# Kernel tuning notes

Measured on AMD Instinct MI355X. Metric: run time of the kernel, lower is better.

The kernel has to match this reference:

```python
import jax, jax.numpy as jnp
import numpy as np

N, R, E, H, F = 50000, 6, 32768, 256, 16
NH, HD = 8, 32
EPS_LN = 1e-5

def _ln(x, g, b):
    mu = x.mean(-1, keepdims=True)
    var = ((x - mu) ** 2).mean(-1, keepdims=True)
    return (x - mu) * jax.lax.rsqrt(var + EPS_LN) * g + b

def setup_inputs() -> dict:
    key = jax.random.key(0)
    ks = jax.random.split(key, 32)
    s = lambda i, shape, scale=0.05: jax.random.normal(ks[i], shape, jnp.float32) * scale
    return {
        'x': jax.random.normal(ks[0], (N, H), jnp.float32),
        'edge_index': jax.random.randint(ks[1], (R, 2, E), 0, N, jnp.int32),
        'edge_attr': jax.random.normal(ks[2], (R, E, F), jnp.float32),
        'Wq': s(3, (R, H, H)), 'bq': s(4, (R, H)),
        'Wk': s(5, (R, H + F, H)), 'bk': s(6, (R, H)),
        'Wv': s(7, (R, H + F, H)), 'bv': s(8, (R, H)),
        'prior': jnp.ones((R, NH), jnp.float32),
        'Wm': s(9, (R, H, H)), 'bm': s(10, (R, H)),
        'W_ir1': s(11, (R * H, H)), 'b_ir1': s(12, (H,)),
        'W_ir2': s(13, (H, R)), 'b_ir2': s(14, (R,)),
        'Wmp': s(15, (3, H, H)), 'bmp': s(16, (3, H)),
        'Wa1': s(17, (H, H // 2)), 'ba1': s(18, (H // 2,)),
        'Wa2': s(19, (H // 2, 1)),
        'g_meta': jnp.ones((H,), jnp.float32), 'b_meta': jnp.zeros((H,), jnp.float32),
        'Wc': s(20, (2 * H, H)), 'bc': s(21, (H,)),
        'g_out': jnp.ones((H,), jnp.float32), 'b_out': jnp.zeros((H,), jnp.float32),
    }

def _block(x, edge_index, edge_attr, Wq, bq, Wk, bk, Wv, bv, prior, Wm, bm,
           W_ir1, b_ir1, W_ir2, b_ir2, Wmp, bmp, Wa1, ba1, Wa2, g_meta, b_meta,
           Wc, bc, g_out, b_out):
    def rel_layer(eidx, eattr, wq, bq_, wk, bk_, wv, bv_, pr, wm, bm_):
        src, dst = eidx[0], eidx[1]
        q = x @ wq + bq_                                  # [N,H]
        kv_in = jnp.concatenate([x[src], eattr], -1)      # [E,H+F]
        k = (kv_in @ wk + bk_).reshape(E, NH, HD)
        v = (kv_in @ wv + bv_).reshape(E, NH, HD)
        qe = q[dst].reshape(E, NH, HD)
        scores = (qe * k).sum(-1) / np.sqrt(HD) * pr      # [E,NH]
        m = jax.ops.segment_max(scores, dst, num_segments=N)
        ex = jnp.exp(scores - m[dst])
        denom = jax.ops.segment_sum(ex, dst, num_segments=N)
        w = ex / (denom[dst] + 1e-16)
        wv_flat = (w[..., None] * v).reshape(E, H)
        agg = jax.ops.segment_sum(wv_flat, dst, num_segments=N)  # [N,H]
        return jax.nn.gelu(agg @ wm + bm_, approximate=False)

    rel_out = jax.vmap(rel_layer)(edge_index, edge_attr, Wq, bq, Wk, bk, Wv, bv,
                                  prior, Wm, bm)          # [R,N,H]

    all_rel = jnp.transpose(rel_out, (1, 0, 2)).reshape(N, R * H)
    h = jax.nn.gelu(all_rel @ W_ir1 + b_ir1, approximate=False)
    inter_w = jax.nn.softmax(h @ W_ir2 + b_ir2, axis=-1)  # [N,R]
    inter_agg = jnp.einsum('nr,rnh->nh', inter_w, rel_out)

    # meta-paths: 0=entangle(ENTANGLE=2,SWAP=3) 1=control(CONTROL=4,ROTATION=0) 2=local(PAULI=1,TEMPORAL=5)
    paths = jnp.stack([rel_out[2] + rel_out[3], rel_out[4] + rel_out[0],
                       rel_out[1] + rel_out[5]], axis=1)  # [N,3,H]
    stacked = jnp.einsum('nph,phk->npk', paths, Wmp) + bmp
    attn = jax.nn.softmax((jnp.tanh(stacked @ Wa1 + ba1) @ Wa2).squeeze(-1), axis=1)
    meta = _ln((attn[..., None] * stacked).sum(1), g_meta, b_meta)

    combined = jax.nn.gelu(jnp.concatenate([inter_agg, meta], -1) @ Wc + bc,
                           approximate=False)
    return _ln(x + combined, g_out, b_out)

def reference(x, edge_index, edge_attr, Wq, bq, Wk, bk, Wv, bv, prior, Wm, bm,
              W_ir1, b_ir1, W_ir2, b_ir2, Wmp, bmp, Wa1, ba1, Wa2, g_meta, b_meta,
              Wc, bc, g_out, b_out):
    return _block(x, edge_index, edge_attr, Wq, bq, Wk, bk, Wv, bv, prior, Wm, bm,
                  W_ir1, b_ir1, W_ir2, b_ir2, Wmp, bmp, Wa1, ba1, Wa2,
                  g_meta, b_meta, Wc, bc, g_out, b_out)
```

## Files before the change

kernel.cpp:

```cpp
#include <hip/hip_runtime.h>
#include <hip/hip_bf16.h>

typedef __hip_bfloat16 bf16;
typedef __attribute__((ext_vector_type(8))) short short8;
typedef __attribute__((ext_vector_type(4))) float f32x4;

#define NN 50000
#define RR 6
#define EE 32768
#define HH 256
#define FF 16
#define NHEAD 8
#define KVP 320

struct __align__(8) bf16x4 { bf16 v[4]; };

__device__ __forceinline__ float b2f(bf16 v) { return __bfloat162float(v); }
__device__ __forceinline__ bf16 f2b(float v) { return __float2bfloat16(v); }
__device__ __forceinline__ short f2s(float f) { bf16 b = f2b(f); return __builtin_bit_cast(short, b); }
__device__ __forceinline__ float s2f(short s) { return b2f(__builtin_bit_cast(bf16, s)); }
__device__ __forceinline__ float gelu_f(float x) { return 0.5f * x * (1.0f + erff(x * 0.7071067811865476f)); }

__device__ __forceinline__ void gl2lds16(const void* g, void* l) {
  __builtin_amdgcn_global_load_lds(
      (const __attribute__((address_space(1))) unsigned int*)g,
      (__attribute__((address_space(3))) unsigned int*)l, 16, 0, 0);
}

__global__ void zero_k(uint4* __restrict__ p, int n16)
{
  const uint4 z = make_uint4(0u, 0u, 0u, 0u);
  for (int i = blockIdx.x * blockDim.x + threadIdx.x; i < n16; i += gridDim.x * blockDim.x)
    p[i] = z;
}

__global__ void cvt_k(const float* __restrict__ in, bf16* __restrict__ out, int n4)
{
  const int i = blockIdx.x * 256 + threadIdx.x;
  if (i >= n4) return;
  const float4 f = ((const float4*)in)[i];
  bf16x4 o; o.v[0] = f2b(f.x); o.v[1] = f2b(f.y); o.v[2] = f2b(f.z); o.v[3] = f2b(f.w);
  ((bf16x4*)out)[i] = o;
}

__global__ void tconv_k(const float* __restrict__ in, bf16* __restrict__ out,
                        int K, int NC, int Kp, long izs, long ozs)
{
  __shared__ float t[32][33];
  in  += (size_t)blockIdx.z * izs;
  out += (size_t)blockIdx.z * ozs;
  const int kb = blockIdx.x * 32, nb = blockIdx.y * 32;
  const int tx = threadIdx.x & 31, ty = threadIdx.x >> 5;
  for (int i = ty; i < 32; i += 8) {
    const int k = kb + i, n = nb + tx;
    t[i][tx] = (k < K && n < NC) ? in[(size_t)k * NC + n] : 0.f;
  }
  __syncthreads();
  for (int i = ty; i < 32; i += 8) {
    const int n = nb + i, k = kb + tx;
    if (n < NC && k < Kp) out[(size_t)n * Kp + k] = f2b(t[tx][i]);
  }
}

__global__ void bkv_k(const float* __restrict__ bk, const float* __restrict__ bv,
                      float* __restrict__ bkv)
{
  const int i = blockIdx.x * 256 + threadIdx.x;
  if (i >= RR * 512) return;
  const int r = i >> 9, c = i & 511;
  bkv[i] = (c < 256) ? bk[r * 256 + c] : bv[r * 256 + (c - 256)];
}

__global__ void copyslot_k(const bf16* __restrict__ tmp, bf16* __restrict__ slot)
{
  const int i = blockIdx.x * 256 + threadIdx.x;
  if (i >= NN * 32) return;
  const int n = i >> 5, c = (i & 31) * 8;
  *(short8*)(slot + (size_t)n * 1536 + c) = *(const short8*)(tmp + (size_t)n * 256 + c);
}

template<int ASRC, int ACT, int ZMODE, typename TO>
__global__ __launch_bounds__(256) void mm_k(
    const void* __restrict__ Av, const bf16* __restrict__ A2, int lda,
    const int* __restrict__ src, const bf16* __restrict__ eab,
    const float* __restrict__ dnm,
    const bf16* __restrict__ Bt, const float* __restrict__ bias,
    const float* __restrict__ wa2, TO* __restrict__ C, int ldc,
    float* __restrict__ logits, int M, int K, int z0)
{
  __shared__ short lA[128 * 64];
  __shared__ short lB[128 * 64];
  const int tid = threadIdx.x;
  const int w = tid >> 6, l = tid & 63;
  const int col0 = blockIdx.x << 7;
  const int row0 = blockIdx.y << 7;
  const bf16* Ab = (const bf16*)Av;
  const bf16* A2b = A2;
  const bf16* Btz = Bt;
  const float* biasz = bias;
  TO* Cz = C;
  float* lg = logits;
  if constexpr (ZMODE == 1) {
    const int slots3[3] = {2, 4, 1};
    Ab = (const bf16*)Av + slots3[blockIdx.z] * 256;
    lg = logits + (size_t)blockIdx.z * M;
  } else if constexpr (ZMODE == 3) {
    const int r1s[3] = {2, 4, 1}, r2s[3] = {3, 0, 5};
    const int z = blockIdx.z + z0;
    Ab  = (const bf16*)Av + (size_t)r1s[z] * 256;
    A2b = A2 + (size_t)r2s[z] * 256;
    Btz = Bt + (size_t)z * 256 * K;
    biasz = bias + z * 256;
    Cz = C + (size_t)blockIdx.z * (size_t)M * 256;
  }
  const int wm = (w >> 1) << 6, wn = (w & 1) << 6;
  const int lane15 = l & 15, kq = l >> 4;

  f32x4 acc[4][4] = {};

  for (int k0 = 0; k0 < K; k0 += 64) {
#pragma unroll
    for (int i = 0; i < 4; ++i) {
      const int idx = (w * 4 + i) * 64 + l;
      const int row = idx >> 3, cg = idx & 7;
      const int scg = cg ^ (row & 7);
      const int r = min(row0 + row, M - 1);
      const int kc = k0 + scg * 8;
      if constexpr (ASRC == 0) {
        gl2lds16(Ab + (size_t)r * lda + kc, &lA[idx * 8]);
      } else if constexpr (ASRC == 2) {
        const short8 u  = *(const short8*)(Ab  + (size_t)r * lda + kc);
        const short8 v2 = *(const short8*)(A2b + (size_t)r * lda + kc);
        short8 s;
#pragma unroll
        for (int j = 0; j < 8; ++j) s[j] = f2s(s2f(u[j]) + s2f(v2[j]));
        *(short8*)&lA[idx * 8] = s;
      } else if constexpr (ASRC == 3) {
        short8 s;
        if (kc < HH) {
          s = *(const short8*)((const bf16*)Av + (size_t)src[r] * HH + kc);
        } else if (kc < HH + FF) {
          s = *(const short8*)(eab + (size_t)r * FF + (kc - HH));
        } else {
#pragma unroll
          for (int j = 0; j < 8; ++j) s[j] = 0;
        }
        *(short8*)&lA[idx * 8] = s;
      } else {
        const float* p = (const float*)Av + (size_t)r * lda + kc;
        const float4 f0 = *(const float4*)p;
        const float4 f1 = *(const float4*)(p + 4);
        const float iv = 1.0f / (dnm[r * NHEAD + (kc >> 5)] + 1e-16f);
        short8 s;
        s[0] = f2s(f0.x * iv); s[1] = f2s(f0.y * iv); s[2] = f2s(f0.z * iv); s[3] = f2s(f0.w * iv);
        s[4] = f2s(f1.x * iv); s[5] = f2s(f1.y * iv); s[6] = f2s(f1.z * iv); s[7] = f2s(f1.w * iv);
        *(short8*)&lA[idx * 8] = s;
      }
    }
#pragma unroll
    for (int i = 0; i < 4; ++i) {
      const int idx = (w * 4 + i) * 64 + l;
      const int row = idx >> 3, cg = idx & 7;
      const int scg = cg ^ (row & 7);
      gl2lds16(Btz + (size_t)(col0 + row) * K + k0 + scg * 8, &lB[idx * 8]);
    }
    __syncthreads();
#pragma unroll
    for (int kk = 0; kk < 64; kk += 32) {
      short8 af[4], bfr[4];
#pragma unroll
      for (int t = 0; t < 4; ++t) {
        const int ra = wm + t * 16 + lane15;
        const int ca = ((kk >> 3) + kq) ^ (ra & 7);
        af[t] = *(const short8*)&lA[ra * 64 + ca * 8];
        const int rb = wn + t * 16 + lane15;
        const int cb = ((kk >> 3) + kq) ^ (rb & 7);
        bfr[t] = *(const short8*)&lB[rb * 64 + cb * 8];
      }
#pragma unroll
      for (int ti = 0; ti < 4; ++ti)
#pragma unroll
        for (int tj = 0; tj < 4; ++tj)
          acc[ti][tj] = __builtin_amdgcn_mfma_f32_16x16x32_bf16(af[ti], bfr[tj], acc[ti][tj], 0, 0, 0);
    }
    __syncthreads();
  }

  if constexpr (ZMODE != 1) {
#pragma unroll
    for (int ti = 0; ti < 4; ++ti) {
#pragma unroll
      for (int reg = 0; reg < 4; ++reg) {
        const int row = row0 + wm + ti * 16 + kq * 4 + reg;
        if (row >= M) continue;
#pragma unroll
        for (int tj = 0; tj < 4; ++tj) {
          const int col = col0 + wn + tj * 16 + lane15;
          float v = acc[ti][tj][reg] + biasz[col];
          if constexpr (ACT == 1) v = gelu_f(v);
          if constexpr (sizeof(TO) == 2) Cz[(size_t)row * ldc + col] = (TO)f2b(v);
          else                           Cz[(size_t)row * ldc + col] = (TO)v;
        }
      }
    }
  } else {
#pragma unroll
    for (int ti = 0; ti < 4; ++ti) {
#pragma unroll
      for (int reg = 0; reg < 4; ++reg) {
        float part = 0.f;
#pragma unroll
        for (int tj = 0; tj < 4; ++tj) {
          const int col = col0 + wn + tj * 16 + lane15;
          part += tanhf(acc[ti][tj][reg] + biasz[col]) * wa2[col];
        }
#pragma unroll
        for (int off = 8; off > 0; off >>= 1) part += __shfl_xor(part, off, 64);
        const int row = row0 + wm + ti * 16 + kq * 4 + reg;
        if (lane15 == 0 && row < M) atomicAdd(&lg[row], part);
      }
    }
  }
}

__global__ void edge_k(const bf16* __restrict__ q, const bf16* __restrict__ kv,
                       const int* __restrict__ dst_idx, const float* __restrict__ prior_r,
                       float* __restrict__ denom, float* __restrict__ agg)
{
  const int e = blockIdx.x, t = threadIdx.x;
  const int dst = dst_idx[e];
  const int h = t >> 5;
  float p = b2f(q[(size_t)dst * 1536 + t]) * b2f(kv[(size_t)e * 512 + t]);
#pragma unroll
  for (int off = 16; off > 0; off >>= 1) p += __shfl_down(p, off, 32);
  const float s = __shfl(p, 0, 32);
  const float ex = expf(s * 0.1767766952966369f * prior_r[h]);
  if ((t & 31) == 0) atomicAdd(&denom[dst * NHEAD + h], ex);
  atomicAdd(&agg[(size_t)dst * HH + t], ex * b2f(kv[(size_t)e * 512 + 256 + t]));
}

__global__ void interw_k(const bf16* __restrict__ h, const float* __restrict__ W2,
                         const float* __restrict__ b2, float* __restrict__ interw)
{
  const int wv = threadIdx.x >> 6, ln = threadIdx.x & 63;
  const int n = blockIdx.x * 4 + wv;
  if (n >= NN) return;
  float a[6] = {0.f, 0.f, 0.f, 0.f, 0.f, 0.f};
#pragma unroll
  for (int kq = 0; kq < 4; ++kq) {
    const int k = ln + (kq << 6);
    const float hv = b2f(h[(size_t)n * HH + k]);
#pragma unroll
    for (int j = 0; j < 6; ++j) a[j] += hv * W2[k * 6 + j];
  }
#pragma unroll
  for (int j = 0; j < 6; ++j) {
#pragma unroll
    for (int off = 32; off > 0; off >>= 1) a[j] += __shfl_down(a[j], off, 64);
  }
  if (ln == 0) {
    float lg[6], e[6], mx = -1e30f, s = 0.f;
#pragma unroll
    for (int j = 0; j < 6; ++j) { lg[j] = a[j] + b2[j]; mx = fmaxf(mx, lg[j]); }
#pragma unroll
    for (int j = 0; j < 6; ++j) { e[j] = expf(lg[j] - mx); s += e[j]; }
    const float inv = 1.0f / s;
#pragma unroll
    for (int j = 0; j < 6; ++j) interw[(size_t)n * 6 + j] = e[j] * inv;
  }
}

__global__ void interagg_k(const float* __restrict__ interw, const bf16* __restrict__ rel_cat,
                           bf16* __restrict__ comb)
{
  const int n = blockIdx.x, t = threadIdx.x;
  float acc = 0.f;
#pragma unroll
  for (int r = 0; r < 6; ++r)
    acc += interw[(size_t)n * 6 + r] * b2f(rel_cat[(size_t)n * 1536 + r * 256 + t]);
  comb[(size_t)n * 512 + t] = f2b(acc);
}

__global__ void metafinal_k(const float* __restrict__ logits, const bf16* __restrict__ rel_cat,
                            const float* __restrict__ gmeta, const float* __restrict__ bmeta,
                            bf16* __restrict__ comb)
{
  const int wv = threadIdx.x >> 6, ln = threadIdx.x & 63;
  const int n = blockIdx.x * 4 + wv;
  if (n >= NN) return;
  const float l0 = logits[n], l1 = logits[NN + n], l2 = logits[2 * NN + n];
  const float mx = fmaxf(l0, fmaxf(l1, l2));
  const float e0 = expf(l0 - mx), e1 = expf(l1 - mx), e2 = expf(l2 - mx);
  const float inv = 1.0f / (e0 + e1 + e2);
  const float a0 = e0 * inv, a1 = e1 * inv, a2 = e2 * inv;
  const size_t base = (size_t)n * 1536;
  float pre[4], s = 0.f, s2 = 0.f;
#pragma unroll
  for (int q4 = 0; q4 < 4; ++q4) {
    const int j = ln + (q4 << 6);
    const float v = a0 * b2f(rel_cat[base + 2 * 256 + j])
                  + a1 * b2f(rel_cat[base + 4 * 256 + j])
                  + a2 * b2f(rel_cat[base + 1 * 256 + j]);
    pre[q4] = v; s += v; s2 += v * v;
  }
#pragma unroll
  for (int off = 32; off > 0; off >>= 1) { s += __shfl_down(s, off, 64); s2 += __shfl_down(s2, off, 64); }
  s = __shfl(s, 0, 64); s2 = __shfl(s2, 0, 64);
  const float mu = s * (1.0f / 256.0f);
  const float var = s2 * (1.0f / 256.0f) - mu * mu;
  const float rs = rsqrtf(var + 1e-5f);
#pragma unroll
  for (int q4 = 0; q4 < 4; ++q4) {
    const int j = ln + (q4 << 6);
    comb[(size_t)n * 512 + 256 + j] = f2b((pre[q4] - mu) * rs * gmeta[j] + bmeta[j]);
  }
}

__global__ void final_k(const float* __restrict__ x, const float* __restrict__ combined,
                        const float* __restrict__ g, const float* __restrict__ b,
                        float* __restrict__ out)
{
  __shared__ float sred[8];
  const int n = blockIdx.x, t = threadIdx.x;
  const float v = x[(size_t)n * HH + t] + combined[(size_t)n * HH + t];
  float s = v, s2 = v * v;
#pragma unroll
  for (int off = 32; off > 0; off >>= 1) { s += __shfl_down(s, off, 64); s2 += __shfl_down(s2, off, 64); }
  const int wv = t >> 6;
  if ((t & 63) == 0) { sred[wv] = s; sred[4 + wv] = s2; }
  __syncthreads();
  const float st = sred[0] + sred[1] + sred[2] + sred[3];
  const float st2 = sred[4] + sred[5] + sred[6] + sred[7];
  const float mu = st * (1.0f / 256.0f);
  const float var = st2 * (1.0f / 256.0f) - mu * mu;
  const float rs = rsqrtf(var + 1e-5f);
  out[(size_t)n * HH + t] = (v - mu) * rs * g[t] + b[t];
}

extern "C" void kernel_launch(void* const* d_in, const int* in_sizes, int n_in,
                              void* d_out, int out_size, void* d_ws, size_t ws_size,
                              hipStream_t stream)
{
  const float* x      = (const float*)d_in[0];
  const int*   eidx   = (const int*)d_in[1];
  const float* eattr  = (const float*)d_in[2];
  const float* Wq     = (const float*)d_in[3];
  const float* bq     = (const float*)d_in[4];
  const float* Wk     = (const float*)d_in[5];
  const float* bk     = (const float*)d_in[6];
  const float* Wv     = (const float*)d_in[7];
  const float* bv     = (const float*)d_in[8];
  const float* prior  = (const float*)d_in[9];
  const float* Wm     = (const float*)d_in[10];
  const float* bm     = (const float*)d_in[11];
  const float* W_ir1  = (const float*)d_in[12];
  const float* b_ir1  = (const float*)d_in[13];
  const float* W_ir2  = (const float*)d_in[14];
  const float* b_ir2  = (const float*)d_in[15];
  const float* Wmp    = (const float*)d_in[16];
  const float* bmp    = (const float*)d_in[17];
  const float* Wa1    = (const float*)d_in[18];
  const float* ba1    = (const float*)d_in[19];
  const float* Wa2    = (const float*)d_in[20];
  const float* g_meta = (const float*)d_in[21];
  const float* b_meta = (const float*)d_in[22];
  const float* Wc     = (const float*)d_in[23];
  const float* bc     = (const float*)d_in[24];
  const float* g_out  = (const float*)d_in[25];
  const float* b_out  = (const float*)d_in[26];
  float* out = (float*)d_out;

  char* ws = (char*)d_ws;
  bf16* rel_cat = (bf16*)ws;
  char* W0 = ws + 153600000;
  bf16*  Wqt   = (bf16*)(W0 + 0);
  bf16*  Wkvt  = (bf16*)(W0 + 786432);
  bf16*  Wmt   = (bf16*)(W0 + 2752512);
  bf16*  Wir1t = (bf16*)(W0 + 3538944);
  bf16*  Wct   = (bf16*)(W0 + 4325376);
  bf16*  Wmpt  = (bf16*)(W0 + 4587520);
  bf16*  Wa1t  = (bf16*)(W0 + 4980736);
  float* bkv   = (float*)(W0 + 5046272);
  char* region = ws + 158658560;
  bf16*     kvbuf = (bf16*)(region + 0);
  float*    denom = (float*)(region + 33554432);
  bf16*     xb    = (bf16*)(region + 38851584);
  bf16*     eab   = (bf16*)(region + 64451584);
  float*    agg   = out;
  bf16*  hbuf     = (bf16*)(region + 0);
  float* interw   = (float*)(region + 33554432);
  bf16*  tmp      = (bf16*)(region + 0);
  float* logits   = (float*)(region + 51200000);
  bf16*  comb     = (bf16*)out;
  float* combined = (float*)(region + 0);

  const dim3 gN(2, 391);
  const dim3 gQ(12, 391);
  const dim3 gKV(4, 256);
  const dim3 gMP2(2, 391, 2);
  const dim3 gMP1(2, 391, 1);
  const dim3 gL(1, 391, 3);

  tconv_k<<<dim3(8, 8, 6), 256, 0, stream>>>(Wq, Wqt, 256, 256, 256, 256 * 256, 256 * 256);
  tconv_k<<<dim3(10, 8, 6), 256, 0, stream>>>(Wk, Wkvt, 272, 256, 320, 272 * 256, 512 * 320);
  tconv_k<<<dim3(10, 8, 6), 256, 0, stream>>>(Wv, Wkvt + 256 * 320, 272, 256, 320, 272 * 256, 512 * 320);
  tconv_k<<<dim3(8, 8, 6), 256, 0, stream>>>(Wm, Wmt, 256, 256, 256, 256 * 256, 256 * 256);
  tconv_k<<<dim3(48, 8, 1), 256, 0, stream>>>(W_ir1, Wir1t, 1536, 256, 1536, 0, 0);
  tconv_k<<<dim3(16, 8, 1), 256, 0, stream>>>(Wc, Wct, 512, 256, 512, 0, 0);
  tconv_k<<<dim3(8, 8, 3), 256, 0, stream>>>(Wmp, Wmpt, 256, 256, 256, 256 * 256, 256 * 256);
  tconv_k<<<dim3(8, 4, 1), 256, 0, stream>>>(Wa1, Wa1t, 256, 128, 256, 0, 0);
  bkv_k<<<12, 256, 0, stream>>>(bk, bv, bkv);
  cvt_k<<<(NN * 64 + 255) / 256, 256, 0, stream>>>(x, xb, NN * 64);
  cvt_k<<<(RR * EE * FF / 4 + 255) / 256, 256, 0, stream>>>(eattr, eab, RR * EE * FF / 4);

  mm_k<0, 0, 0, bf16><<<gQ, 256, 0, stream>>>(
      xb, nullptr, 256, nullptr, nullptr, nullptr,
      Wqt, bq, nullptr, rel_cat, 1536, nullptr, NN, 256, 0);

  for (int r = 0; r < RR; ++r) {
    const int* src = eidx + (size_t)r * 2 * EE;
    const int* dst = src + EE;
    zero_k<<<98, 256, 0, stream>>>((uint4*)denom, (NN * NHEAD * 4) / 16);
    zero_k<<<2048, 256, 0, stream>>>((uint4*)agg, (NN * HH * 4) / 16);
    mm_k<3, 0, 0, bf16><<<gKV, 256, 0, stream>>>(
        xb, nullptr, 0, src, eab + (size_t)r * EE * FF, nullptr,
        Wkvt + (size_t)r * 512 * KVP, bkv + r * 512, nullptr, kvbuf, 512, nullptr, EE, KVP, 0);
    edge_k<<<EE, 256, 0, stream>>>(rel_cat + r * 256, kvbuf, dst, prior + r * NHEAD, denom, agg);
    mm_k<4, 1, 0, bf16><<<gN, 256, 0, stream>>>(
        agg, nullptr, 256, nullptr, nullptr, denom,
        Wmt + (size_t)r * 256 * 256, bm + r * HH, nullptr,
        rel_cat + r * 256, 1536, nullptr, NN, 256, 0);
  }

  mm_k<0, 1, 0, bf16><<<gN, 256, 0, stream>>>(
      rel_cat, nullptr, 1536, nullptr, nullptr, nullptr,
      Wir1t, b_ir1, nullptr, hbuf, 256, nullptr, NN, 1536, 0);
  interw_k<<<(NN + 3) / 4, 256, 0, stream>>>(hbuf, W_ir2, b_ir2, interw);
  interagg_k<<<NN, 256, 0, stream>>>(interw, rel_cat, comb);

  mm_k<2, 0, 3, bf16><<<gMP2, 256, 0, stream>>>(
      rel_cat, rel_cat, 1536, nullptr, nullptr, nullptr,
      Wmpt, bmp, nullptr, tmp, 256, nullptr, NN, 256, 0);
  copyslot_k<<<(NN * 32 + 255) / 256, 256, 0, stream>>>(tmp, rel_cat + 2 * 256);
  copyslot_k<<<(NN * 32 + 255) / 256, 256, 0, stream>>>(tmp + (size_t)NN * 256, rel_cat + 4 * 256);
  mm_k<2, 0, 3, bf16><<<gMP1, 256, 0, stream>>>(
      rel_cat, rel_cat, 1536, nullptr, nullptr, nullptr,
      Wmpt, bmp, nullptr, tmp, 256, nullptr, NN, 256, 2);
  copyslot_k<<<(NN * 32 + 255) / 256, 256, 0, stream>>>(tmp, rel_cat + 1 * 256);

  zero_k<<<147, 256, 0, stream>>>((uint4*)logits, (3 * NN * 4) / 16);
  mm_k<0, 0, 1, bf16><<<gL, 256, 0, stream>>>(
      rel_cat, nullptr, 1536, nullptr, nullptr, nullptr,
      Wa1t, ba1, Wa2, (bf16*)nullptr, 0, logits, NN, 256, 0);
  metafinal_k<<<(NN + 3) / 4, 256, 0, stream>>>(logits, rel_cat, g_meta, b_meta, comb);

  mm_k<0, 1, 0, float><<<gN, 256, 0, stream>>>(
      comb, nullptr, 512, nullptr, nullptr, nullptr,
      Wct, bc, nullptr, combined, 256, nullptr, NN, 512, 0);
  final_k<<<NN, 256, 0, stream>>>(x, combined, g_out, b_out, out);
}
```

Measured before the change: 1.442 ms.

## Double-buffer LDS tiles in GEMM kernel to overlap global loads with MFMA

Turns the shared GEMM kernel's main loop into a two-stage software pipeline. LDS A/B tiles become double buffers, and the next K-tile is prefetched while MFMAs run on the current one, with explicit vmcnt waits and barriers in place of __syncthreads. The gathered-edge path (ASRC 3) now uses direct global-to-LDS loads, reading a zeroed pad buffer for the K padding. This doubles LDS use to 64KB per block, which can lower occupancy, and relies on hand-counted vmcnt values being correct.

New measurement: 1.485 ms. +3.0%, slower.

```diff
diff --git a/kernel.cpp b/kernel.cpp
--- a/kernel.cpp
+++ b/kernel.cpp
@@ -88,8 +88,8 @@
     const float* __restrict__ wa2, TO* __restrict__ C, int ldc,
     float* __restrict__ logits, int M, int K, int z0)
 {
-  __shared__ short lA[128 * 64];
-  __shared__ short lB[128 * 64];
+  __shared__ short lA[2][128 * 64];
+  __shared__ short lB[2][128 * 64];
   const int tid = threadIdx.x;
   const int w = tid >> 6, l = tid & 63;
   const int col0 = blockIdx.x << 7;
@@ -116,66 +116,103 @@
   const int wm = (w >> 1) << 6, wn = (w & 1) << 6;
   const int lane15 = l & 15, kq = l >> 4;
 
+  int idx8[4], rowic[4], scg8[4], ri[4], si[4];
+#pragma unroll
+  for (int i = 0; i < 4; ++i) {
+    const int idx = (w * 4 + i) * 64 + l;
+    rowic[i] = idx >> 3;
+    scg8[i]  = ((idx & 7) ^ (rowic[i] & 7)) * 8;
+    idx8[i]  = idx * 8;
+    ri[i]    = min(row0 + rowic[i], M - 1);
+    if constexpr (ASRC == 3) si[i] = src[ri[i]];
+  }
+
+  short8 ps[4], ps2[4]; float4 pf[8];
+
+  auto stageB = [&](int t, int b) {
+#pragma unroll
+    for (int i = 0; i < 4; ++i)
+      gl2lds16(Btz + (size_t)(col0 + rowic[i]) * K + (t << 6) + scg8[i], &lB[b][idx8[i]]);
+  };
+  auto stageA = [&](int t, int b) {
+    const int k0 = t << 6;
+#pragma unroll
+    for (int i = 0; i < 4; ++i) {
+      const int kc = k0 + scg8[i];
+      if constexpr (ASRC == 0) {
+        gl2lds16(Ab + (size_t)ri[i] * lda + kc, &lA[b][idx8[i]]);
+      } else if constexpr (ASRC == 3) {
+        const bf16* p = (kc < HH) ? (const bf16*)Av + (size_t)si[i] * HH + kc
+                      : (kc < HH + FF) ? eab + (size_t)ri[i] * FF + (kc - HH)
+                      : (const bf16*)dnm;
+        gl2lds16(p, &lA[b][idx8[i]]);
+      } else if constexpr (ASRC == 2) {
+        ps[i]  = *(const short8*)(Ab  + (size_t)ri[i] * lda + kc);
+        ps2[i] = *(const short8*)(A2b + (size_t)ri[i] * lda + kc);
+      } else {
+        const float* p = (const float*)Av + (size_t)ri[i] * lda + kc;
+        pf[2 * i] = *(const float4*)p; pf[2 * i + 1] = *(const float4*)(p + 4);
+      }
+    }
+  };
+  auto writeA = [&](int t, int b) {
+    const int k0 = t << 6;
+    if constexpr (ASRC == 2) {
+#pragma unroll
+      for (int i = 0; i < 4; ++i) {
+        short8 s;
+#pragma unroll
+        for (int j = 0; j < 8; ++j) s[j] = f2s(s2f(ps[i][j]) + s2f(ps2[i][j]));
+        *(short8*)&lA[b][idx8[i]] = s;
+      }
+    } else if constexpr (ASRC == 4) {
+#pragma unroll
+      for (int i = 0; i < 4; ++i) {
+        const int kc = k0 + scg8[i];
+        const float iv = 1.0f / (dnm[ri[i] * NHEAD + (kc >> 5)] + 1e-16f);
+        short8 s;
+        s[0] = f2s(pf[2*i].x * iv); s[1] = f2s(pf[2*i].y * iv);
+        s[2] = f2s(pf[2*i].z * iv); s[3] = f2s(pf[2*i].w * iv);
+        s[4] = f2s(pf[2*i+1].x * iv); s[5] = f2s(pf[2*i+1].y * iv);
+        s[6] = f2s(pf[2*i+1].z * iv); s[7] = f2s(pf[2*i+1].w * iv);
+        *(short8*)&lA[b][idx8[i]] = s;
+      }
+    }
+  };
+
   f32x4 acc[4][4] = {};
-
-  for (int k0 = 0; k0 < K; k0 += 64) {
-#pragma unroll
-    for (int i = 0; i < 4; ++i) {
-      const int idx = (w * 4 + i) * 64 + l;
-      const int row = idx >> 3, cg = idx & 7;
-      const int scg = cg ^ (row & 7);
-      const int r = min(row0 + row, M - 1);
-      const int kc = k0 + scg * 8;
-      if constexpr (ASRC == 0) {
-        gl2lds16(Ab + (size_t)r * lda + kc, &lA[idx * 8]);
-      } else if constexpr (ASRC == 2) {
-        const short8 u  = *(const short8*)(Ab  + (size_t)r * lda + kc);
-        const short8 v2 = *(const short8*)(A2b + (size_t)r * lda + kc);
-        short8 s;
-#pragma unroll
-        for (int j = 0; j < 8; ++j) s[j] = f2s(s2f(u[j]) + s2f(v2[j]));
-        *(short8*)&lA[idx * 8] = s;
-      } else if constexpr (ASRC == 3) {
-        short8 s;
-        if (kc < HH) {
-          s = *(const short8*)((const bf16*)Av + (size_t)src[r] * HH + kc);
-        } else if (kc < HH + FF) {
-          s = *(const short8*)(eab + (size_t)r * FF + (kc - HH));
-        } else {
-#pragma unroll
-          for (int j = 0; j < 8; ++j) s[j] = 0;
-        }
-        *(short8*)&lA[idx * 8] = s;
-      } else {
-        const float* p = (const float*)Av + (size_t)r * lda + kc;
-        const float4 f0 = *(const float4*)p;
-        const float4 f1 = *(const float4*)(p + 4);
-        const float iv = 1.0f / (dnm[r * NHEAD + (kc >> 5)] + 1e-16f);
-        short8 s;
-        s[0] = f2s(f0.x * iv); s[1] = f2s(f0.y * iv); s[2] = f2s(f0.z * iv); s[3] = f2s(f0.w * iv);
-        s[4] = f2s(f1.x * iv); s[5] = f2s(f1.y * iv); s[6] = f2s(f1.z * iv); s[7] = f2s(f1.w * iv);
-        *(short8*)&lA[idx * 8] = s;
-      }
-    }
-#pragma unroll
-    for (int i = 0; i < 4; ++i) {
-      const int idx = (w * 4 + i) * 64 + l;
-      const int row = idx >> 3, cg = idx & 7;
-      const int scg = cg ^ (row & 7);
-      gl2lds16(Btz + (size_t)(col0 + row) * K + k0 + scg * 8, &lB[idx * 8]);
-    }
-    __syncthreads();
+  const int NT = K >> 6;
+
+  stageA(0, 0);
+  stageB(0, 0);
+  if constexpr (ASRC == 2 || ASRC == 4) writeA(0, 0);
+
+  int cur = 0;
+  for (int t = 0; t < NT; ++t) {
+    const int nb = cur ^ 1;
+    if (t + 1 < NT) {
+      stageA(t + 1, nb);
+      stageB(t + 1, nb);
+      if constexpr (ASRC == 0 || ASRC == 3)
+        asm volatile("s_waitcnt vmcnt(8) lgkmcnt(0)" ::: "memory");
+      else
+        asm volatile("s_waitcnt vmcnt(12) lgkmcnt(0)" ::: "memory");
+    } else {
+      asm volatile("s_waitcnt vmcnt(0) lgkmcnt(0)" ::: "memory");
+    }
+    __builtin_amdgcn_s_barrier();
+    __builtin_amdgcn_sched_barrier(0);
 #pragma unroll
     for (int kk = 0; kk < 64; kk += 32) {
       short8 af[4], bfr[4];
 #pragma unroll
-      for (int t = 0; t < 4; ++t) {
-        const int ra = wm + t * 16 + lane15;
+      for (int tt = 0; tt < 4; ++tt) {
+        const int ra = wm + tt * 16 + lane15;
         const int ca = ((kk >> 3) + kq) ^ (ra & 7);
-        af[t] = *(const short8*)&lA[ra * 64 + ca * 8];
-        const int rb = wn + t * 16 + lane15;
+        af[tt] = *(const short8*)&lA[cur][ra * 64 + ca * 8];
+        const int rb = wn + tt * 16 + lane15;
         const int cb = ((kk >> 3) + kq) ^ (rb & 7);
-        bfr[t] = *(const short8*)&lB[rb * 64 + cb * 8];
+        bfr[tt] = *(const short8*)&lB[cur][rb * 64 + cb * 8];
       }
 #pragma unroll
       for (int ti = 0; ti < 4; ++ti)
@@ -183,7 +220,13 @@
         for (int tj = 0; tj < 4; ++tj)
           acc[ti][tj] = __builtin_amdgcn_mfma_f32_16x16x32_bf16(af[ti], bfr[tj], acc[ti][tj], 0, 0, 0);
     }
-    __syncthreads();
+    if (t + 1 < NT) {
+      if constexpr (ASRC == 2 || ASRC == 4) writeA(t + 1, nb);
+      asm volatile("s_waitcnt lgkmcnt(0)" ::: "memory");
+      __builtin_amdgcn_s_barrier();
+      __builtin_amdgcn_sched_barrier(0);
+    }
+    cur = nb;
   }
 
   if constexpr (ZMODE != 1) {
@@ -386,6 +429,7 @@
   float*    denom = (float*)(region + 33554432);
   bf16*     xb    = (bf16*)(region + 38851584);
   bf16*     eab   = (bf16*)(region + 64451584);
+  bf16*     zpad  = (bf16*)(region + 70743040);
   float*    agg   = out;
   bf16*  hbuf     = (bf16*)(region + 0);
   float* interw   = (float*)(region + 33554432);
@@ -412,6 +456,7 @@
   bkv_k<<<12, 256, 0, stream>>>(bk, bv, bkv);
   cvt_k<<<(NN * 64 + 255) / 256, 256, 0, stream>>>(x, xb, NN * 64);
   cvt_k<<<(RR * EE * FF / 4 + 255) / 256, 256, 0, stream>>>(eattr, eab, RR * EE * FF / 4);
+  zero_k<<<1, 256, 0, stream>>>((uint4*)zpad, 4);
 
   mm_k<0, 0, 0, bf16><<<gQ, 256, 0, stream>>>(
       xb, nullptr, 256, nullptr, nullptr, nullptr,
@@ -423,7 +468,7 @@
     zero_k<<<98, 256, 0, stream>>>((uint4*)denom, (NN * NHEAD * 4) / 16);
     zero_k<<<2048, 256, 0, stream>>>((uint4*)agg, (NN * HH * 4) / 16);
     mm_k<3, 0, 0, bf16><<<gKV, 256, 0, stream>>>(
-        xb, nullptr, 0, src, eab + (size_t)r * EE * FF, nullptr,
+        xb, nullptr, 0, src, eab + (size_t)r * EE * FF, (const float*)zpad,
         Wkvt + (size_t)r * 512 * KVP, bkv + r * 512, nullptr, kvbuf, 512, nullptr, EE, KVP, 0);
     edge_k<<<EE, 256, 0, stream>>>(rel_cat + r * 256, kvbuf, dst, prior + r * NHEAD, denom, agg);
     mm_k<4, 1, 0, bf16><<<gN, 256, 0, stream>>>(
```

## Fuse attention scores and softmax denominators into KV GEMM epilogue, batch relation pairs

Applied to the files above, without the earlier changes.

The K/V projection GEMM now computes the per-edge attention scores in its epilogue. Blocks covering K columns gather q[dst] into LDS, form per-head dot products, exponentiate, store exp scores and atomically add the denominators. Blocks covering V columns write only V, which shrinks the edge kernel to a weighted scatter-add of V. Relations are processed in pairs via blockIdx.z to raise GEMM occupancy and cut launches, at the cost of a larger workspace and extra gathers of q rows inside the GEMM.

New measurement: 1.458 ms. Within noise of the previous version (+1.1%).

```diff
diff --git a/kernel.cpp b/kernel.cpp
--- a/kernel.cpp
+++ b/kernel.cpp
@@ -88,8 +88,7 @@
     const float* __restrict__ wa2, TO* __restrict__ C, int ldc,
     float* __restrict__ logits, int M, int K, int z0)
 {
-  __shared__ short lA[128 * 64];
-  __shared__ short lB[128 * 64];
+  __shared__ short lds[2 * 128 * 64];
   const int tid = threadIdx.x;
   const int w = tid >> 6, l = tid & 63;
   const int col0 = blockIdx.x << 7;
@@ -100,6 +99,13 @@
   const float* biasz = bias;
   TO* Cz = C;
   float* lg = logits;
+  const int* srcz = src;
+  const int* dstz = nullptr;
+  const bf16* eabz = eab;
+  const bf16* qz = nullptr;
+  float* exbz = nullptr;
+  float* dnmaz = nullptr;
+  const float* priz = nullptr;
   if constexpr (ZMODE == 1) {
     const int slots3[3] = {2, 4, 1};
     Ab = (const bf16*)Av + slots3[blockIdx.z] * 256;
@@ -112,6 +118,18 @@
     Btz = Bt + (size_t)z * 256 * K;
     biasz = bias + z * 256;
     Cz = C + (size_t)blockIdx.z * (size_t)M * 256;
+  } else if constexpr (ZMODE == 4) {
+    const int z = blockIdx.z;
+    srcz  = src + (size_t)z * 2 * EE;
+    dstz  = srcz + EE;
+    eabz  = eab + (size_t)z * EE * FF;
+    qz    = A2 + z * 256;
+    Btz   = Bt + (size_t)z * 512 * KVP;
+    biasz = bias + z * 512;
+    Cz    = C + (size_t)z * (size_t)EE * 256;
+    exbz  = logits + (size_t)z * EE * NHEAD;
+    dnmaz = logits + (size_t)2 * EE * NHEAD + (size_t)z * NN * NHEAD;
+    priz  = dnm + z * NHEAD;
   }
   const int wm = (w >> 1) << 6, wn = (w & 1) << 6;
   const int lane15 = l & 15, kq = l >> 4;
@@ -127,25 +145,25 @@
       const int r = min(row0 + row, M - 1);
       const int kc = k0 + scg * 8;
       if constexpr (ASRC == 0) {
-        gl2lds16(Ab + (size_t)r * lda + kc, &lA[idx * 8]);
+        gl2lds16(Ab + (size_t)r * lda + kc, &lds[idx * 8]);
       } else if constexpr (ASRC == 2) {
         const short8 u  = *(const short8*)(Ab  + (size_t)r * lda + kc);
         const short8 v2 = *(const short8*)(A2b + (size_t)r * lda + kc);
         short8 s;
 #pragma unroll
         for (int j = 0; j < 8; ++j) s[j] = f2s(s2f(u[j]) + s2f(v2[j]));
-        *(short8*)&lA[idx * 8] = s;
+        *(short8*)&lds[idx * 8] = s;
       } else if constexpr (ASRC == 3) {
         short8 s;
         if (kc < HH) {
-          s = *(const short8*)((const bf16*)Av + (size_t)src[r] * HH + kc);
+          s = *(const short8*)((const bf16*)Av + (size_t)srcz[r] * HH + kc);
         } else if (kc < HH + FF) {
-          s = *(const short8*)(eab + (size_t)r * FF + (kc - HH));
+          s = *(const short8*)(eabz + (size_t)r * FF + (kc - HH));
         } else {
 #pragma unroll
           for (int j = 0; j < 8; ++j) s[j] = 0;
         }
-        *(short8*)&lA[idx * 8] = s;
+        *(short8*)&lds[idx * 8] = s;
       } else {
         const float* p = (const float*)Av + (size_t)r * lda + kc;
         const float4 f0 = *(const float4*)p;
@@ -154,7 +172,7 @@
         short8 s;
         s[0] = f2s(f0.x * iv); s[1] = f2s(f0.y * iv); s[2] = f2s(f0.z * iv); s[3] = f2s(f0.w * iv);
         s[4] = f2s(f1.x * iv); s[5] = f2s(f1.y * iv); s[6] = f2s(f1.z * iv); s[7] = f2s(f1.w * iv);
-        *(short8*)&lA[idx * 8] = s;
+        *(short8*)&lds[idx * 8] = s;
       }
     }
 #pragma unroll
@@ -162,7 +180,7 @@
       const int idx = (w * 4 + i) * 64 + l;
       const int row = idx >> 3, cg = idx & 7;
       const int scg = cg ^ (row & 7);
-      gl2lds16(Btz + (size_t)(col0 + row) * K + k0 + scg * 8, &lB[idx * 8]);
+      gl2lds16(Btz + (size_t)(col0 + row) * K + k0 + scg * 8, &lds[8192 + idx * 8]);
     }
     __syncthreads();
 #pragma unroll
@@ -172,10 +190,10 @@
       for (int t = 0; t < 4; ++t) {
         const int ra = wm + t * 16 + lane15;
         const int ca = ((kk >> 3) + kq) ^ (ra & 7);
-        af[t] = *(const short8*)&lA[ra * 64 + ca * 8];
+        af[t] = *(const short8*)&lds[ra * 64 + ca * 8];
         const int rb = wn + t * 16 + lane15;
         const int cb = ((kk >> 3) + kq) ^ (rb & 7);
-        bfr[t] = *(const short8*)&lB[rb * 64 + cb * 8];
+        bfr[t] = *(const short8*)&lds[8192 + rb * 64 + cb * 8];
       }
 #pragma unroll
       for (int ti = 0; ti < 4; ++ti)
@@ -186,7 +204,64 @@
     __syncthreads();
   }
 
-  if constexpr (ZMODE != 1) {
+  if constexpr (ZMODE == 4) {
+    if (blockIdx.x < 2) {
+#pragma unroll
+      for (int i = 0; i < 8; ++i) {
+        const int idx = (w * 8 + i) * 64 + l;
+        const int row = idx >> 4, cg = idx & 15;
+        const int d = dstz[row0 + row];
+        gl2lds16(qz + (size_t)d * 1536 + col0 + cg * 8, &lds[idx * 8]);
+      }
+      __syncthreads();
+      const int hb = (col0 + wn) >> 5;
+      const float pr0 = priz[hb], pr1 = priz[hb + 1];
+#pragma unroll
+      for (int ti = 0; ti < 4; ++ti) {
+#pragma unroll
+        for (int reg = 0; reg < 4; ++reg) {
+          const int row = wm + ti * 16 + kq * 4 + reg;
+          float p0 = 0.f, p1 = 0.f;
+#pragma unroll
+          for (int tj = 0; tj < 4; ++tj) {
+            const int colL = wn + tj * 16 + lane15;
+            const float kv_ = acc[ti][tj][reg] + biasz[col0 + colL];
+            const float qv = s2f(lds[(row << 7) + colL]);
+            if (tj < 2) p0 += qv * kv_; else p1 += qv * kv_;
+          }
+#pragma unroll
+          for (int off = 1; off < 16; off <<= 1) {
+            p0 += __shfl_xor(p0, off, 64);
+            p1 += __shfl_xor(p1, off, 64);
+          }
+          if (lane15 == 0) {
+            const int e = row0 + row;
+            const int d = dstz[e];
+            const float e0 = expf(p0 * 0.1767766952966369f * pr0);
+            const float e1 = expf(p1 * 0.1767766952966369f * pr1);
+            exbz[e * NHEAD + hb]     = e0;
+            exbz[e * NHEAD + hb + 1] = e1;
+            atomicAdd(&dnmaz[d * NHEAD + hb],     e0);
+            atomicAdd(&dnmaz[d * NHEAD + hb + 1], e1);
+          }
+        }
+      }
+    } else {
+#pragma unroll
+      for (int ti = 0; ti < 4; ++ti) {
+#pragma unroll
+        for (int reg = 0; reg < 4; ++reg) {
+          const int row = row0 + wm + ti * 16 + kq * 4 + reg;
+#pragma unroll
+          for (int tj = 0; tj < 4; ++tj) {
+            const int col = col0 + wn + tj * 16 + lane15;
+            const float v = acc[ti][tj][reg] + biasz[col];
+            Cz[(size_t)row * 256 + (col - 256)] = (TO)f2b(v);
+          }
+        }
+      }
+    }
+  } else if constexpr (ZMODE != 1) {
 #pragma unroll
     for (int ti = 0; ti < 4; ++ti) {
 #pragma unroll
@@ -223,20 +298,13 @@
   }
 }
 
-__global__ void edge_k(const bf16* __restrict__ q, const bf16* __restrict__ kv,
-                       const int* __restrict__ dst_idx, const float* __restrict__ prior_r,
-                       float* __restrict__ denom, float* __restrict__ agg)
+__global__ void edge2_k(const float* __restrict__ ex, const bf16* __restrict__ v,
+                        const int* __restrict__ dst_idx, float* __restrict__ agg)
 {
   const int e = blockIdx.x, t = threadIdx.x;
   const int dst = dst_idx[e];
-  const int h = t >> 5;
-  float p = b2f(q[(size_t)dst * 1536 + t]) * b2f(kv[(size_t)e * 512 + t]);
-#pragma unroll
-  for (int off = 16; off > 0; off >>= 1) p += __shfl_down(p, off, 32);
-  const float s = __shfl(p, 0, 32);
-  const float ex = expf(s * 0.1767766952966369f * prior_r[h]);
-  if ((t & 31) == 0) atomicAdd(&denom[dst * NHEAD + h], ex);
-  atomicAdd(&agg[(size_t)dst * HH + t], ex * b2f(kv[(size_t)e * 512 + 256 + t]));
+  const float w = ex[e * NHEAD + (t >> 5)];
+  atomicAdd(&agg[(size_t)dst * HH + t], w * b2f(v[(size_t)e * HH + t]));
 }
 
 __global__ void interw_k(const bf16* __restrict__ h, const float* __restrict__ W2,
@@ -382,11 +450,12 @@
   bf16*  Wa1t  = (bf16*)(W0 + 4980736);
   float* bkv   = (float*)(W0 + 5046272);
   char* region = ws + 158658560;
-  bf16*     kvbuf = (bf16*)(region + 0);
-  float*    denom = (float*)(region + 33554432);
-  bf16*     xb    = (bf16*)(region + 38851584);
-  bf16*     eab   = (bf16*)(region + 64451584);
-  float*    agg   = out;
+  bf16*  kvbuf  = (bf16*)(region + 0);
+  float* exden  = (float*)(region + 33554432);
+  float* denom2 = exden + 2 * EE * NHEAD;
+  bf16*  xb     = (bf16*)(region + 38851584);
+  bf16*  eab    = (bf16*)(region + 64451584);
+  float* agg    = out;
   bf16*  hbuf     = (bf16*)(region + 0);
   float* interw   = (float*)(region + 33554432);
   bf16*  tmp      = (bf16*)(region + 0);
@@ -396,7 +465,7 @@
 
   const dim3 gN(2, 391);
   const dim3 gQ(12, 391);
-  const dim3 gKV(4, 256);
+  const dim3 gKV(4, 256, 2);
   const dim3 gMP2(2, 391, 2);
   const dim3 gMP1(2, 391, 1);
   const dim3 gL(1, 391, 3);
@@ -417,19 +486,26 @@
       xb, nullptr, 256, nullptr, nullptr, nullptr,
       Wqt, bq, nullptr, rel_cat, 1536, nullptr, NN, 256, 0);
 
-  for (int r = 0; r < RR; ++r) {
-    const int* src = eidx + (size_t)r * 2 * EE;
-    const int* dst = src + EE;
-    zero_k<<<98, 256, 0, stream>>>((uint4*)denom, (NN * NHEAD * 4) / 16);
-    zero_k<<<2048, 256, 0, stream>>>((uint4*)agg, (NN * HH * 4) / 16);
-    mm_k<3, 0, 0, bf16><<<gKV, 256, 0, stream>>>(
-        xb, nullptr, 0, src, eab + (size_t)r * EE * FF, nullptr,
-        Wkvt + (size_t)r * 512 * KVP, bkv + r * 512, nullptr, kvbuf, 512, nullptr, EE, KVP, 0);
-    edge_k<<<EE, 256, 0, stream>>>(rel_cat + r * 256, kvbuf, dst, prior + r * NHEAD, denom, agg);
-    mm_k<4, 1, 0, bf16><<<gN, 256, 0, stream>>>(
-        agg, nullptr, 256, nullptr, nullptr, denom,
-        Wmt + (size_t)r * 256 * 256, bm + r * HH, nullptr,
-        rel_cat + r * 256, 1536, nullptr, NN, 256, 0);
+  for (int pr = 0; pr < 3; ++pr) {
+    const int r0 = 2 * pr;
+    zero_k<<<391, 256, 0, stream>>>((uint4*)denom2, (2 * NN * NHEAD * 4) / 16);
+    mm_k<3, 0, 4, bf16><<<gKV, 256, 0, stream>>>(
+        xb, rel_cat + r0 * 256, 0,
+        eidx + (size_t)r0 * 2 * EE, eab + (size_t)r0 * EE * FF,
+        prior + r0 * NHEAD,
+        Wkvt + (size_t)r0 * 512 * KVP, bkv + r0 * 512, nullptr,
+        kvbuf, 256, exden, EE, KVP, 0);
+    for (int j = 0; j < 2; ++j) {
+      const int r = r0 + j;
+      const int* dst = eidx + (size_t)r * 2 * EE + EE;
+      zero_k<<<2048, 256, 0, stream>>>((uint4*)agg, (NN * HH * 4) / 16);
+      edge2_k<<<EE, 256, 0, stream>>>(
+          exden + (size_t)j * EE * NHEAD, kvbuf + (size_t)j * EE * 256, dst, agg);
+      mm_k<4, 1, 0, bf16><<<gN, 256, 0, stream>>>(
+          agg, nullptr, 256, nullptr, nullptr, denom2 + (size_t)j * NN * NHEAD,
+          Wmt + (size_t)r * 256 * 256, bm + r * HH, nullptr,
+          rel_cat + r * 256, 1536, nullptr, NN, 256, 0);
+    }
   }
 
   mm_k<0, 1, 0, bf16><<<gN, 256, 0, stream>>>(
```
